# Performance work log

Hardware: AMD Instinct MI355X
Metric: run time of the kernel (lower is better)

Reference implementation:

```python
import jax, jax.numpy as jnp
import numpy as np

B, N = 16384, 4096
NBLOCKS = 4
BLK = N // NBLOCKS  # 1024


def setup_inputs() -> dict:
    key = jax.random.key(0)
    kx, k1, k2, kb = jax.random.split(key, 4)
    # match torch kaiming-style uniform bounds approximately; exact init values
    # don't affect correctness testing, scale kept modest for stability
    bound_w = float(np.sqrt(3.0) * (np.sqrt(2.0 / (1 + 5)) / np.sqrt(BLK)))
    bound_b = 1.0 / float(np.sqrt(N))
    x = jax.random.normal(kx, (B, N), dtype=jnp.float32)
    w1 = jax.random.uniform(k1, (NBLOCKS, BLK, BLK), jnp.float32, -bound_w, bound_w)
    w2 = jax.random.uniform(k2, (NBLOCKS, BLK, BLK), jnp.float32, -bound_w, bound_w)
    bias = jax.random.uniform(kb, (N,), jnp.float32, -bound_b, bound_b)
    return {"x": x, "w1": w1, "w2": w2, "bias": bias}


def monarch_matmul(x, w1, w2):
    # x: (B, n); w1: (k, q, p) with k*p = n; w2: (l, s, r) with l*r = k*q
    Bd, n = x.shape
    k, q, p = w1.shape
    l, s, r = w2.shape
    # out1[b,k,q] = sum_p x[b,k,p] * w1[k,q,p]
    out1 = jnp.einsum('bkp,kqp->bkq', x.reshape(Bd, k, p), w1)
    # permute (k*q) flat -> (r, l), then transpose to (l, r)
    t = out1.reshape(Bd, r, l).transpose(0, 2, 1)  # (B, l, r)
    # out2[b,l,s] = sum_r t[b,l,r] * w2[l,s,r]
    out2 = jnp.einsum('blr,lsr->bls', t, w2)
    # permute to (B, s, l) then flatten -> (B, s*l)
    return out2.transpose(0, 2, 1).reshape(Bd, s * l)


def reference(x, w1, w2, bias):
    return monarch_matmul(x, w1, w2) + bias
```

## Files before the change

kernel.cpp:

```cpp
#include <hip/hip_runtime.h>
#include <hip/hip_bf16.h>
#include <stdint.h>

typedef __bf16 bf16_t;
typedef bf16_t bf16x8 __attribute__((ext_vector_type(8)));
typedef bf16_t bf16x4 __attribute__((ext_vector_type(4)));
typedef float  f32x4  __attribute__((ext_vector_type(4)));

#define B_DIM 16384

#define BARM()   asm volatile("s_barrier" ::: "memory")
#define SCHED0() __builtin_amdgcn_sched_barrier(0)
#define LGKM0()  asm volatile("s_waitcnt lgkmcnt(0)" ::: "memory")
#define VMCNT6() asm volatile("s_waitcnt vmcnt(6)" ::: "memory")
#define VMCNT0() asm volatile("s_waitcnt vmcnt(0)" ::: "memory")

__device__ __forceinline__ void async_copy16(void* lptr, const void* gptr) {
  __builtin_amdgcn_global_load_lds(
      (const __attribute__((address_space(1))) unsigned int*)gptr,
      (__attribute__((address_space(3))) unsigned int*)lptr, 16, 0, 0);
}

__global__ void cast_all_kernel(const float* __restrict__ x, const float* __restrict__ w1,
                                const float* __restrict__ w2, bf16_t* __restrict__ xb,
                                bf16_t* __restrict__ w1b, bf16_t* __restrict__ w2b) {
  size_t c = (size_t)blockIdx.x * 256 + threadIdx.x;
  const float* s; bf16_t* d; size_t off;
  if (c < 8388608)      { s = x;  d = xb;  off = c; }
  else if (c < 8912896) { s = w1; d = w1b; off = c - 8388608; }
  else                  { s = w2; d = w2b; off = c - 8912896; }
  size_t i = off * 8;
  f32x4 a = *(const f32x4*)(s + i);
  f32x4 b = *(const f32x4*)(s + i + 4);
  bf16x8 o;
  o[0]=(bf16_t)a[0]; o[1]=(bf16_t)a[1]; o[2]=(bf16_t)a[2]; o[3]=(bf16_t)a[3];
  o[4]=(bf16_t)b[0]; o[5]=(bf16_t)b[1]; o[6]=(bf16_t)b[2]; o[7]=(bf16_t)b[3];
  *(bf16x8*)(d + i) = o;
}

template<int EPI>
__global__ __launch_bounds__(512, 2)
void monarch_gemm8(const bf16_t* __restrict__ Ab, const bf16_t* __restrict__ Wb,
                   bf16_t* __restrict__ Outb)
{
  __shared__ __align__(16) char smem[131072];
  const int tid  = threadIdx.x;
  const int lane = tid & 63;
  const int wid  = tid >> 6;
  const int wm   = wid >> 2;
  const int wn   = wid & 3;

  const int pb = blockIdx.x;
  const int lb = (pb & 7) * 128 + (pb >> 3);
  const int zi = lb >> 8;
  const int mt = (lb & 255) >> 2;
  const int nt = lb & 3;

  const size_t brow0 = (size_t)mt * 256;
  const int    ncol0 = nt * 256;

  const bf16_t* Asrc = Ab + brow0 * 4096 + (size_t)zi * 1024;
  const bf16_t* Bsrc = Wb + ((size_t)zi << 20) + (size_t)ncol0 * 1024;

  const int sRow = lane >> 3;
  const int sC   = (lane & 7) ^ sRow;

  auto stage = [&](int t, int h) {
    const int ldsBase = (t & 1) * 65536 + (h >> 1) * 32768 + (h & 1) * 16384;
    const bf16_t* src = (h < 2) ? (Asrc + (size_t)(h * 128) * 4096 + t * 64)
                                : (Bsrc + (size_t)((h - 2) * 128) * 1024 + t * 64);
    const size_t strideE = (h < 2) ? 4096 : 1024;
    #pragma unroll
    for (int j = 0; j < 2; ++j) {
      const int row = j * 64 + wid * 8 + sRow;
      async_copy16(smem + ldsBase + j * 8192 + wid * 1024,
                   src + (size_t)row * strideE + sC * 8);
    }
  };

  const int cs0 = ((0 + (lane >> 4)) ^ (lane & 7)) * 16;
  const int cs1 = ((4 + (lane >> 4)) ^ (lane & 7)) * 16;
  const int aBase = (wm * 128 + (lane & 15)) * 128;
  const int bBase = 32768 + (wn * 64 + (lane & 15)) * 128;

#define RDA(buf, m, kk) (*(const bf16x8*)(smem + (buf)*65536 + aBase + (m)*2048 + ((kk)?cs1:cs0)))
#define RDB(buf, n, kk) (*(const bf16x8*)(smem + (buf)*65536 + bBase + (n)*2048 + ((kk)?cs1:cs0)))

  f32x4 acc[8][4] = {};
  bf16x8 aM0[4][2], aM1[4][2], bN0[2][2], bN1[2][2];

#define MFMA_QUAD(AR, Aarr, NB, Barr)                                              \
  __builtin_amdgcn_s_setprio(1);                                                   \
  _Pragma("unroll") for (int m = 0; m < 4; ++m)                                    \
  _Pragma("unroll") for (int n = 0; n < 2; ++n)                                    \
  _Pragma("unroll") for (int kk = 0; kk < 2; ++kk)                                 \
    acc[(AR)+m][(NB)+n] = __builtin_amdgcn_mfma_f32_16x16x32_bf16(                 \
        Aarr[m][kk], Barr[n][kk], acc[(AR)+m][(NB)+n], 0, 0, 0);                   \
  __builtin_amdgcn_s_setprio(0);

#define LD_A0(buf) _Pragma("unroll") for (int m = 0; m < 4; ++m) { \
    aM0[m][0] = RDA(buf,m,0); aM0[m][1] = RDA(buf,m,1); }
#define LD_A1(buf) _Pragma("unroll") for (int m = 0; m < 4; ++m) { \
    aM1[m][0] = RDA(buf,m+4,0); aM1[m][1] = RDA(buf,m+4,1); }
#define LD_B0(buf) _Pragma("unroll") for (int n = 0; n < 2; ++n) { \
    bN0[n][0] = RDB(buf,n,0); bN0[n][1] = RDB(buf,n,1); }
#define LD_B1(buf) _Pragma("unroll") for (int n = 0; n < 2; ++n) { \
    bN1[n][0] = RDB(buf,n+2,0); bN1[n][1] = RDB(buf,n+2,1); }

  stage(0,0); stage(0,1); stage(0,2); stage(0,3);
  stage(1,0); stage(1,1); stage(1,2);
  VMCNT6(); BARM();
  LD_B0(0);

  for (int it2 = 0; it2 < 8; ++it2) {
    const int t0 = it2 * 2;
    const bool notlast = (it2 < 7);
    LD_A0(0);
    stage(t0+1, 3);
    BARM(); LGKM0(); SCHED0();
    MFMA_QUAD(0, aM0, 0, bN0);
    BARM();
    LD_A1(0);
    BARM(); LGKM0(); SCHED0();
    MFMA_QUAD(4, aM1, 0, bN0);
    BARM();
    LD_B1(0);
    if (notlast) stage(t0+2, 0);
    BARM(); LGKM0(); SCHED0();
    MFMA_QUAD(0, aM0, 2, bN1);
    BARM();
    if (notlast) { stage(t0+2, 1); stage(t0+2, 2); VMCNT6(); }
    else         { VMCNT0(); }
    BARM();
    LD_B0(1);
    MFMA_QUAD(4, aM1, 2, bN1);
    BARM();
    LD_A0(1);
    if (notlast) stage(t0+2, 3);
    BARM(); LGKM0(); SCHED0();
    MFMA_QUAD(0, aM0, 0, bN0);
    BARM();
    LD_A1(1);
    BARM(); LGKM0(); SCHED0();
    MFMA_QUAD(4, aM1, 0, bN0);
    BARM();
    LD_B1(1);
    if (notlast) stage(t0+3, 0);
    BARM(); LGKM0(); SCHED0();
    MFMA_QUAD(0, aM0, 2, bN1);
    BARM();
    if (notlast) { stage(t0+3, 1); stage(t0+3, 2); VMCNT6(); }
    BARM();
    if (notlast) { LD_B0(0); }
    MFMA_QUAD(4, aM1, 2, bN1);
    BARM();
  }

  bf16_t* C = (bf16_t*)smem;
  #pragma unroll
  for (int half = 0; half < 2; ++half) {
    BARM();
    if (wm == half) {
      const int rg = lane >> 4, cl = lane & 15;
      #pragma unroll
      for (int m = 0; m < 8; ++m)
        #pragma unroll
        for (int n = 0; n < 4; ++n) {
          const int rl = m * 16 + rg * 4;
          const int col = wn * 64 + n * 16 + cl;
          #pragma unroll
          for (int j = 0; j < 4; ++j)
            C[(rl + j) * 264 + col] = (bf16_t)acc[m][n][j];
        }
    }
    BARM();
    if (EPI == 0) {
      #pragma unroll
      for (int i = 0; i < 8; ++i) {
        const int s = i * 512 + tid;
        const int row = s >> 5, l = (s >> 3) & 3, part = s & 7;
        bf16x8 v;
        #pragma unroll
        for (int u = 0; u < 8; ++u) v[u] = C[row * 264 + l + 4 * (part * 8 + u)];
        *(bf16x8*)&Outb[(brow0 + half * 128 + row) * 4096 +
                        l * 1024 + zi * 256 + nt * 64 + part * 8] = v;
      }
    } else {
      #pragma unroll
      for (int i = 0; i < 8; ++i) {
        const int s = i * 512 + tid;
        const int row = s >> 5, ch = s & 31;
        bf16x8 v = *(const bf16x8*)&C[row * 264 + ch * 8];
        *(bf16x8*)&Outb[(brow0 + half * 128 + row) * 4096 +
                        (size_t)zi * 1024 + ncol0 + ch * 8] = v;
      }
    }
  }
#undef RDA
#undef RDB
#undef MFMA_QUAD
#undef LD_A0
#undef LD_A1
#undef LD_B0
#undef LD_B1
}

__global__ void permute_bias_kernel(const bf16_t* __restrict__ o2,
                                    const float* __restrict__ bias,
                                    float* __restrict__ out) {
  const int t = blockIdx.x * 256 + threadIdx.x;
  const int b = t >> 8;
  const int s0 = (t & 255) * 4;
  const size_t rowb = (size_t)b * 4096;
  bf16x4 vl[4];
  #pragma unroll
  for (int l = 0; l < 4; ++l) vl[l] = *(const bf16x4*)(o2 + rowb + l * 1024 + s0);
  #pragma unroll
  for (int si = 0; si < 4; ++si) {
    f32x4 bb = *(const f32x4*)(bias + (size_t)(s0 + si) * 4);
    f32x4 o;
    o[0] = (float)vl[0][si] + bb[0];
    o[1] = (float)vl[1][si] + bb[1];
    o[2] = (float)vl[2][si] + bb[2];
    o[3] = (float)vl[3][si] + bb[3];
    *(f32x4*)(out + rowb + (size_t)(s0 + si) * 4) = o;
  }
}

extern "C" void kernel_launch(void* const* d_in, const int* in_sizes, int n_in,
                              void* d_out, int out_size, void* d_ws, size_t ws_size,
                              hipStream_t stream) {
  const float* x    = (const float*)d_in[0];
  const float* w1   = (const float*)d_in[1];
  const float* w2   = (const float*)d_in[2];
  const float* bias = (const float*)d_in[3];
  float* out = (float*)d_out;

  char* ws = (char*)d_ws;
  const size_t xbBytes    = (size_t)B_DIM * 4096 * 2;
  const size_t wBytes     = (size_t)8 << 20;
  bf16_t* xb    = (bf16_t*)(ws);
  bf16_t* w1b   = (bf16_t*)(ws + xbBytes);
  bf16_t* w2b   = (bf16_t*)(ws + xbBytes + wBytes);
  bf16_t* inter = (bf16_t*)(ws + xbBytes + 2 * wBytes);
  bf16_t* o2    = xb;

  cast_all_kernel<<<36864, 256, 0, stream>>>(x, w1, w2, xb, w1b, w2b);
  monarch_gemm8<0><<<1024, 512, 0, stream>>>(xb, w1b, inter);
  monarch_gemm8<1><<<1024, 512, 0, stream>>>(inter, w2b, o2);
  permute_bias_kernel<<<16384, 256, 0, stream>>>(o2, bias, out);
}
```

Measured before the change: 491.6 us.

## Drop explicit LDS waits and pre-permute EPI0 epilogue layout in LDS

Replaces the inline-asm barriers plus explicit lgkmcnt(0) waits and sched_barriers with the compiler builtin barrier and plain memory fences, letting the compiler schedule LDS waits itself. The staging lambda becomes a macro with the buffer index passed explicitly. For the first epilogue variant, accumulators are written into LDS already in the permuted (l, column) order with a padded stride, so the read-back becomes one vectorized 16-byte load instead of eight strided scalar loads. Dropping the explicit waits risks the compiler placing waits less favourably or reordering MFMAs across the phase boundaries.

New measurement: 499.0 us. Within noise of the previous version (+1.5%).

```diff
diff --git a/kernel.cpp b/kernel.cpp
--- a/kernel.cpp
+++ b/kernel.cpp
@@ -9,9 +9,8 @@
 
 #define B_DIM 16384
 
-#define BARM()   asm volatile("s_barrier" ::: "memory")
-#define SCHED0() __builtin_amdgcn_sched_barrier(0)
-#define LGKM0()  asm volatile("s_waitcnt lgkmcnt(0)" ::: "memory")
+#define BAR()    __builtin_amdgcn_s_barrier()
+#define MEMF()   asm volatile("" ::: "memory")
 #define VMCNT6() asm volatile("s_waitcnt vmcnt(6)" ::: "memory")
 #define VMCNT0() asm volatile("s_waitcnt vmcnt(0)" ::: "memory")
 
@@ -65,18 +64,15 @@
   const int sRow = lane >> 3;
   const int sC   = (lane & 7) ^ sRow;
 
-  auto stage = [&](int t, int h) {
-    const int ldsBase = (t & 1) * 65536 + (h >> 1) * 32768 + (h & 1) * 16384;
-    const bf16_t* src = (h < 2) ? (Asrc + (size_t)(h * 128) * 4096 + t * 64)
-                                : (Bsrc + (size_t)((h - 2) * 128) * 1024 + t * 64);
-    const size_t strideE = (h < 2) ? 4096 : 1024;
-    #pragma unroll
-    for (int j = 0; j < 2; ++j) {
-      const int row = j * 64 + wid * 8 + sRow;
-      async_copy16(smem + ldsBase + j * 8192 + wid * 1024,
-                   src + (size_t)row * strideE + sC * 8);
-    }
-  };
+#define STAGE(BUF, T, H) do {                                                   \
+    const bf16_t* _s = (H) < 2 ? Asrc + ((size_t)((H) * 128) * 4096) + (T) * 64 \
+                               : Bsrc + ((size_t)(((H)-2) * 128) * 1024) + (T) * 64; \
+    const size_t _st = (H) < 2 ? 4096 : 1024;                                   \
+    async_copy16(smem + (BUF)*65536 + ((H)>>1)*32768 + ((H)&1)*16384 + wid*1024,\
+                 _s + (size_t)(wid * 8 + sRow) * _st + sC * 8);                 \
+    async_copy16(smem + (BUF)*65536 + ((H)>>1)*32768 + ((H)&1)*16384 + 8192 + wid*1024, \
+                 _s + (size_t)(64 + wid * 8 + sRow) * _st + sC * 8);            \
+  } while (0)
 
   const int cs0 = ((0 + (lane >> 4)) ^ (lane & 7)) * 16;
   const int cs1 = ((4 + (lane >> 4)) ^ (lane & 7)) * 16;
@@ -107,85 +103,102 @@
 #define LD_B1(buf) _Pragma("unroll") for (int n = 0; n < 2; ++n) { \
     bN1[n][0] = RDB(buf,n+2,0); bN1[n][1] = RDB(buf,n+2,1); }
 
-  stage(0,0); stage(0,1); stage(0,2); stage(0,3);
-  stage(1,0); stage(1,1); stage(1,2);
-  VMCNT6(); BARM();
+  STAGE(0,0,0); MEMF(); STAGE(0,0,1); MEMF(); STAGE(0,0,2); MEMF(); STAGE(0,0,3); MEMF();
+  STAGE(1,1,0); MEMF(); STAGE(1,1,1); MEMF(); STAGE(1,1,2);
+  VMCNT6(); BAR();
   LD_B0(0);
 
   for (int it2 = 0; it2 < 8; ++it2) {
     const int t0 = it2 * 2;
-    const bool notlast = (it2 < 7);
+    const bool nl = (it2 < 7);
     LD_A0(0);
-    stage(t0+1, 3);
-    BARM(); LGKM0(); SCHED0();
+    MEMF(); STAGE(1, t0+1, 3);
+    BAR();
     MFMA_QUAD(0, aM0, 0, bN0);
-    BARM();
+    BAR();
     LD_A1(0);
-    BARM(); LGKM0(); SCHED0();
+    BAR();
     MFMA_QUAD(4, aM1, 0, bN0);
-    BARM();
+    BAR();
     LD_B1(0);
-    if (notlast) stage(t0+2, 0);
-    BARM(); LGKM0(); SCHED0();
+    if (nl) { MEMF(); STAGE(0, t0+2, 0); }
+    BAR();
     MFMA_QUAD(0, aM0, 2, bN1);
-    BARM();
-    if (notlast) { stage(t0+2, 1); stage(t0+2, 2); VMCNT6(); }
-    else         { VMCNT0(); }
-    BARM();
+    BAR();
+    if (nl) { MEMF(); STAGE(0, t0+2, 1); MEMF(); STAGE(0, t0+2, 2); VMCNT6(); }
+    else    { VMCNT0(); }
+    BAR();
     LD_B0(1);
     MFMA_QUAD(4, aM1, 2, bN1);
-    BARM();
+    BAR();
     LD_A0(1);
-    if (notlast) stage(t0+2, 3);
-    BARM(); LGKM0(); SCHED0();
+    if (nl) { MEMF(); STAGE(0, t0+2, 3); }
+    BAR();
     MFMA_QUAD(0, aM0, 0, bN0);
-    BARM();
+    BAR();
     LD_A1(1);
-    BARM(); LGKM0(); SCHED0();
+    BAR();
     MFMA_QUAD(4, aM1, 0, bN0);
-    BARM();
+    BAR();
     LD_B1(1);
-    if (notlast) stage(t0+3, 0);
-    BARM(); LGKM0(); SCHED0();
+    if (nl) { MEMF(); STAGE(1, t0+3, 0); }
+    BAR();
     MFMA_QUAD(0, aM0, 2, bN1);
-    BARM();
-    if (notlast) { stage(t0+3, 1); stage(t0+3, 2); VMCNT6(); }
-    BARM();
-    if (notlast) { LD_B0(0); }
+    BAR();
+    if (nl) { MEMF(); STAGE(1, t0+3, 1); MEMF(); STAGE(1, t0+3, 2); VMCNT6(); }
+    BAR();
+    if (nl) { LD_B0(0); }
     MFMA_QUAD(4, aM1, 2, bN1);
-    BARM();
+    BAR();
   }
 
-  bf16_t* C = (bf16_t*)smem;
-  #pragma unroll
-  for (int half = 0; half < 2; ++half) {
-    BARM();
-    if (wm == half) {
-      const int rg = lane >> 4, cl = lane & 15;
-      #pragma unroll
-      for (int m = 0; m < 8; ++m)
+  if (EPI == 0) {
+    bf16_t* C0 = (bf16_t*)smem;
+    #pragma unroll
+    for (int half = 0; half < 2; ++half) {
+      BAR();
+      if (wm == half) {
+        const int rg = lane >> 4, cl = lane & 15;
+        const int l = cl & 3, rvb = cl >> 2;
         #pragma unroll
-        for (int n = 0; n < 4; ++n) {
-          const int rl = m * 16 + rg * 4;
-          const int col = wn * 64 + n * 16 + cl;
+        for (int m = 0; m < 8; ++m)
           #pragma unroll
-          for (int j = 0; j < 4; ++j)
-            C[(rl + j) * 264 + col] = (bf16_t)acc[m][n][j];
-        }
-    }
-    BARM();
-    if (EPI == 0) {
+          for (int n = 0; n < 4; ++n) {
+            const int rowb = (m * 16 + rg * 4) * 288 + l * 72 + wn * 16 + n * 4 + rvb;
+            #pragma unroll
+            for (int j = 0; j < 4; ++j)
+              C0[rowb + j * 288] = (bf16_t)acc[m][n][j];
+          }
+      }
+      BAR();
       #pragma unroll
       for (int i = 0; i < 8; ++i) {
         const int s = i * 512 + tid;
-        const int row = s >> 5, l = (s >> 3) & 3, part = s & 7;
-        bf16x8 v;
+        const int row = s >> 5, l2 = (s >> 3) & 3, part = s & 7;
+        bf16x8 v = *(const bf16x8*)&C0[row * 288 + l2 * 72 + part * 8];
+        *(bf16x8*)&Outb[(brow0 + half * 128 + row) * 4096 +
+                        l2 * 1024 + zi * 256 + nt * 64 + part * 8] = v;
+      }
+    }
+  } else {
+    bf16_t* C = (bf16_t*)smem;
+    #pragma unroll
+    for (int half = 0; half < 2; ++half) {
+      BAR();
+      if (wm == half) {
+        const int rg = lane >> 4, cl = lane & 15;
         #pragma unroll
-        for (int u = 0; u < 8; ++u) v[u] = C[row * 264 + l + 4 * (part * 8 + u)];
-        *(bf16x8*)&Outb[(brow0 + half * 128 + row) * 4096 +
-                        l * 1024 + zi * 256 + nt * 64 + part * 8] = v;
-      }
-    } else {
+        for (int m = 0; m < 8; ++m)
+          #pragma unroll
+          for (int n = 0; n < 4; ++n) {
+            const int rl = m * 16 + rg * 4;
+            const int col = wn * 64 + n * 16 + cl;
+            #pragma unroll
+            for (int j = 0; j < 4; ++j)
+              C[(rl + j) * 264 + col] = (bf16_t)acc[m][n][j];
+          }
+      }
+      BAR();
       #pragma unroll
       for (int i = 0; i < 8; ++i) {
         const int s = i * 512 + tid;
@@ -203,6 +216,7 @@
 #undef LD_A1
 #undef LD_B0
 #undef LD_B1
+#undef STAGE
 }
 
 __global__ void permute_bias_kernel(const bf16_t* __restrict__ o2,
```
